# Optimization experiments

Hardware: AMD Instinct MI355X
Metric: run time of the kernel (lower is better)

The kernel has to match this reference:

```python
import jax, jax.numpy as jnp
import numpy as np
from jax import lax

ALPHA = 100.0          # SuperSpike surrogate slope (method='super', alpha=100)
DT_TAU_MEM = 0.1       # dt * tau_mem_inv = 0.001 * 100
DT_TAU_SYN = 0.2       # dt * tau_syn_inv = 0.001 * 200
V_TH = 1.0
SEQ = 40

@jax.custom_vjp
def spike(x):
    return (x > 0).astype(x.dtype)

def _spike_fwd(x):
    return (x > 0).astype(x.dtype), x

def _spike_bwd(x, g):
    # SuperSpike surrogate gradient: 1 / (alpha*|x| + 1)^2
    return (g / (ALPHA * jnp.abs(x) + 1.0) ** 2,)

spike.defvjp(_spike_fwd, _spike_bwd)

def encode(current):
    # ConstantCurrentLIFEncoder: LIF driven by constant current, SEQ steps.
    def step(v, _):
        v = v + DT_TAU_MEM * (-v + current)   # v_leak = 0
        z = spike(v - V_TH)
        v = v * (1.0 - z)                     # v_reset = 0
        return v, z
    _, zs = lax.scan(step, jnp.zeros_like(current), None, length=SEQ)
    return zs  # (SEQ, B, F)

def setup_inputs() -> dict:
    key = jax.random.key(0)
    ks = jax.random.split(key, 5)
    B = 16384
    x = jax.random.normal(ks[0], (B, 4), jnp.float32)
    w_in = jax.random.normal(ks[1], (128, 8), jnp.float32) * np.sqrt(2.0 / 8)
    w_rec = jax.random.normal(ks[2], (128, 128), jnp.float32) * np.sqrt(2.0 / 128)
    w_out = jax.random.normal(ks[3], (2, 128), jnp.float32) * np.sqrt(2.0 / 128)
    keep = jax.random.bernoulli(ks[4], 0.5, (SEQ, B, 128))
    dropout_mask = keep.astype(jnp.float32) * 2.0  # inverted dropout, p=0.5
    return {"x": x, "w_in": w_in, "w_rec": w_rec, "w_out": w_out,
            "dropout_mask": dropout_mask}

def reference(x, w_in, w_rec, w_out, dropout_mask):
    scale = 50.0
    x_pos = encode(jax.nn.relu(scale * x))     # (T, B, 4)
    x_neg = encode(jax.nn.relu(-scale * x))    # (T, B, 4)
    xs = jnp.concatenate([x_pos, x_neg], axis=2)  # (T, B, 8)

    B = x.shape[0]
    H = w_rec.shape[0]
    O = w_out.shape[0]
    z0 = jnp.zeros((B, H), x.dtype)
    v0 = jnp.zeros((B, H), x.dtype)
    i0 = jnp.zeros((B, H), x.dtype)
    vo0 = jnp.zeros((B, O), x.dtype)
    io0 = jnp.zeros((B, O), x.dtype)

    def step(carry, inp):
        z, v, i, vo, io = carry
        xt, mt = inp
        # LIFCell (recurrent)
        v_dec = v + DT_TAU_MEM * (-v + i)
        i_dec = i * (1.0 - DT_TAU_SYN)
        z_new = spike(v_dec - V_TH)
        v_new = (1.0 - z_new) * v_dec
        i_new = i_dec + xt @ w_in.T + z @ w_rec.T
        # Dropout on spikes
        z_d = z_new * mt
        # LICell readout
        vo_new = vo + DT_TAU_MEM * (-vo + io)
        io_new = io * (1.0 - DT_TAU_SYN) + z_d @ w_out.T
        return (z_new, v_new, i_new, vo_new, io_new), vo_new

    _, voltages = lax.scan(step, (z0, v0, i0, vo0, io0), (xs, dropout_mask))
    m = jnp.max(voltages, axis=0)          # (B, O)
    return jax.nn.softmax(m, axis=1)
```

## Files before the change

kernel.cpp:

```cpp
#include <hip/hip_runtime.h>
#include <cstdint>

#define T_SEQ 40
#define NB    16384
#define NH    128
#define ZSTR  168
#define GROWS 16
#define NTHR  256
#define NBLK  (NB / GROWS)

typedef float v4f __attribute__((ext_vector_type(4)));
typedef short v8s __attribute__((ext_vector_type(8)));

__device__ __forceinline__ unsigned short f2bf(float f) {
  uint32_t u = __float_as_uint(f);
  return (unsigned short)((u + 0x7FFFu + ((u >> 16) & 1u)) >> 16);
}
__device__ __forceinline__ float bf2f(unsigned short b) {
  return __uint_as_float(((uint32_t)b) << 16);
}
template <int C>
__device__ __forceinline__ float dppadd(float v) {
  int t = __builtin_amdgcn_update_dpp(0, __float_as_int(v), C, 0xF, 0xF, true);
  return v + __int_as_float(t);
}
__device__ __forceinline__ float red16(float v) {
  v = dppadd<0x111>(v);
  v = dppadd<0x112>(v);
  v = dppadd<0x114>(v);
  v = dppadd<0x118>(v);
  return v;
}

__global__ __launch_bounds__(NTHR, 2)
void Policy_22033182228693_kernel(const float* __restrict__ x,
                                  const float* __restrict__ w_in,
                                  const float* __restrict__ w_rec,
                                  const float* __restrict__ w_out,
                                  const float* __restrict__ dmask,
                                  float* __restrict__ out)
{
  __shared__ unsigned short Z[2][GROWS * ZSTR];
  __shared__ unsigned short XS[T_SEQ * 128];
  __shared__ float MB[2][GROWS * NH];
  __shared__ float UP[T_SEQ][4][GROWS][2];

  const int tid  = threadIdx.x;
  const int wv   = tid >> 6;
  const int lane = tid & 63;
  const int m    = lane & 15;
  const int q    = lane >> 4;
  const int wcol = wv * 32;
  const int gb   = blockIdx.x * GROWS;
  const size_t TS = (size_t)NB * NH;

  v8s bfr[2][5][3];
#pragma unroll
  for (int tau = 0; tau < 2; ++tau) {
    const int n = wcol + tau * 16 + m;
#pragma unroll
    for (int c = 0; c < 5; ++c) {
      const int kb = c * 32 + q * 8;
      float w8[8];
      if (c < 4) {
        float4 wa = *(const float4*)&w_rec[n * NH + kb];
        float4 wb = *(const float4*)&w_rec[n * NH + kb + 4];
        w8[0]=wa.x; w8[1]=wa.y; w8[2]=wa.z; w8[3]=wa.w;
        w8[4]=wb.x; w8[5]=wb.y; w8[6]=wb.z; w8[7]=wb.w;
      } else if (q == 0) {
        float4 wa = *(const float4*)&w_in[n * 8];
        float4 wb = *(const float4*)&w_in[n * 8 + 4];
        w8[0]=wa.x; w8[1]=wa.y; w8[2]=wa.z; w8[3]=wa.w;
        w8[4]=wb.x; w8[5]=wb.y; w8[6]=wb.z; w8[7]=wb.w;
      } else {
#pragma unroll
        for (int j = 0; j < 8; ++j) w8[j] = 0.f;
      }
      union { v8s v; unsigned short u[8]; } f0, f1, f2;
#pragma unroll
      for (int j = 0; j < 8; ++j) {
        float w = w8[j];
        unsigned short b1 = f2bf(w);  float r1 = w - bf2f(b1);
        unsigned short b2 = f2bf(r1); float r2 = r1 - bf2f(b2);
        unsigned short b3 = f2bf(r2);
        f0.u[j] = b1; f1.u[j] = b2; f2.u[j] = b3;
      }
      bfr[tau][c][0] = f0.v; bfr[tau][c][1] = f1.v; bfr[tau][c][2] = f2.v;
    }
  }

  const float wo00 = w_out[wcol + m],      wo01 = w_out[wcol + 16 + m];
  const float wo10 = w_out[NH + wcol + m], wo11 = w_out[NH + wcol + 16 + m];

  for (int e = tid; e < 2 * GROWS * ZSTR; e += NTHR) ((unsigned short*)Z)[e] = 0;
  __syncthreads();

  const int srow = tid >> 4;
  const int scol = (tid & 15) * 8;
  {
    const float* g0 = dmask + (size_t)(gb + srow) * NH + scol;
    float4 p0 = *(const float4*)g0;
    float4 p1 = *(const float4*)(g0 + 4);
    if (tid < 128) {
      const int bi = tid >> 3, ch = tid & 7;
      float xv = x[(size_t)(gb + bi) * 4 + (ch & 3)];
      float cc = fmaxf(0.f, ((ch & 4) ? -50.f : 50.f) * xv);
      float ve = 0.f;
      for (int t = 0; t < T_SEQ; ++t) {
        ve += 0.1f * (cc - ve);
        unsigned short zb = 0;
        if (ve > 1.0f) { zb = 0x3F80; ve = 0.f; }
        XS[t * 128 + tid] = zb;
        if (t == 0) Z[0][bi * ZSTR + NH + ch] = zb;
      }
    }
    float* mrow = &MB[0][srow * NH + scol];
    *(float4*)mrow = p0;
    *(float4*)(mrow + 4) = p1;
  }
  __syncthreads();

  v4f iacc[2] = {{0,0,0,0},{0,0,0,0}};
  v4f vmem[2] = {{0,0,0,0},{0,0,0,0}};
  int pb = 0;

#pragma unroll 1
  for (int t = 0; t < T_SEQ; ++t) {
    const int tn = (t + 1 < T_SEQ) ? t + 1 : T_SEQ - 1;
    const float* gs = dmask + (size_t)tn * TS + (size_t)(gb + srow) * NH + scol;
    float4 npf0 = *(const float4*)gs;
    float4 npf1 = *(const float4*)(gs + 4);

    v8s af[5];
    const unsigned short* zrow = &Z[pb][m * ZSTR];
#pragma unroll
    for (int c = 0; c < 5; ++c) af[c] = *(const v8s*)(zrow + c * 32 + q * 8);

    float zf[2][4];
#pragma unroll
    for (int tau = 0; tau < 2; ++tau) {
      v4f vd = vmem[tau] + 0.1f * (iacc[tau] - vmem[tau]);
#pragma unroll
      for (int r = 0; r < 4; ++r) {
        bool z = vd[r] > 1.0f;
        zf[tau][r] = z ? 1.0f : 0.0f;
        vmem[tau][r] = z ? 0.0f : vd[r];
      }
    }

    v4f s00 = 0.8f * iacc[0], s01 = {0,0,0,0}, s02 = {0,0,0,0};
    v4f s10 = 0.8f * iacc[1], s11 = {0,0,0,0}, s12 = {0,0,0,0};
#pragma unroll
    for (int c = 0; c < 5; ++c) {
      s00 = __builtin_amdgcn_mfma_f32_16x16x32_bf16(af[c], bfr[0][c][0], s00, 0, 0, 0);
      s10 = __builtin_amdgcn_mfma_f32_16x16x32_bf16(af[c], bfr[1][c][0], s10, 0, 0, 0);
      s01 = __builtin_amdgcn_mfma_f32_16x16x32_bf16(af[c], bfr[0][c][1], s01, 0, 0, 0);
      s11 = __builtin_amdgcn_mfma_f32_16x16x32_bf16(af[c], bfr[1][c][1], s11, 0, 0, 0);
      s02 = __builtin_amdgcn_mfma_f32_16x16x32_bf16(af[c], bfr[0][c][2], s02, 0, 0, 0);
      s12 = __builtin_amdgcn_mfma_f32_16x16x32_bf16(af[c], bfr[1][c][2], s12, 0, 0, 0);
    }
    iacc[0] = (s00 + s01) + s02;
    iacc[1] = (s10 + s11) + s12;

    unsigned short* zq = &Z[pb ^ 1][0];
#pragma unroll
    for (int tau = 0; tau < 2; ++tau)
#pragma unroll
      for (int r = 0; r < 4; ++r)
        zq[(q * 4 + r) * ZSTR + wcol + tau * 16 + m] = (zf[tau][r] != 0.f) ? 0x3F80 : 0;

    if (t + 1 < T_SEQ && tid >= 128) {
      const int u = tid - 128;
      Z[pb ^ 1][(u >> 3) * ZSTR + NH + (u & 7)] = XS[(t + 1) * 128 + u];
    }

#pragma unroll
    for (int r = 0; r < 4; ++r) {
      float mk0 = MB[t & 1][(q * 4 + r) * NH + wcol + m];
      float mk1 = MB[t & 1][(q * 4 + r) * NH + wcol + 16 + m];
      float zd0 = zf[0][r] * mk0;
      float zd1 = zf[1][r] * mk1;
      float p0 = zd0 * wo00 + zd1 * wo01;
      float p1 = zd0 * wo10 + zd1 * wo11;
      p0 = red16(p0);
      p1 = red16(p1);
      if (m == 15) {
        UP[t][wv][q * 4 + r][0] = p0;
        UP[t][wv][q * 4 + r][1] = p1;
      }
    }

    {
      float* mrow = &MB[(t + 1) & 1][srow * NH + scol];
      *(float4*)mrow = npf0;
      *(float4*)(mrow + 4) = npf1;
    }

    __syncthreads();
    pb ^= 1;
  }

  if (tid < 32) {
    const int row = tid >> 1, o = tid & 1;
    float io = 0.f, vo = 0.f, mx = -3.0e38f;
#pragma unroll 1
    for (int t = 0; t < T_SEQ; ++t) {
      float u = ((UP[t][0][row][o] + UP[t][1][row][o])
               +  UP[t][2][row][o]) + UP[t][3][row][o];
      float von = vo + 0.1f * (io - vo);
      io = 0.8f * io + u;
      vo = von;
      mx = fmaxf(mx, vo);
    }
    float other = __shfl_xor(mx, 1);
    if (o == 0) {
      float mxx = fmaxf(mx, other);
      float e0 = expf(mx - mxx), e1 = expf(other - mxx);
      float inv = 1.f / (e0 + e1);
      ((float2*)out)[gb + row] = make_float2(e0 * inv, e1 * inv);
    }
  }
}

extern "C" void kernel_launch(void* const* d_in, const int* in_sizes, int n_in,
                              void* d_out, int out_size, void* d_ws, size_t ws_size,
                              hipStream_t stream) {
  const float* x     = (const float*)d_in[0];
  const float* w_in  = (const float*)d_in[1];
  const float* w_rec = (const float*)d_in[2];
  const float* w_out = (const float*)d_in[3];
  const float* dmask = (const float*)d_in[4];
  float* out = (float*)d_out;

  hipLaunchKernelGGL(Policy_22033182228693_kernel, dim3(NBLK), dim3(NTHR), 0, stream,
                     x, w_in, w_rec, w_out, dmask, out);
}
```

Baseline: 472.4 us.

## Widen blocks to 32 rows and 8 waves, one hidden column tile per wave

Each block now handles 32 batch rows with 512 threads. Each wave owns 16 hidden columns and runs two row tiles, so the split-bf16 weight fragments held in registers are halved and the weight setup is amortised over more rows. The dropout mask is prefetched two steps ahead into a triple buffer with a padded stride, and the readout integration runs inside the step loop on wave 0 using a double-buffered partial array instead of a tail loop over all steps. The costs are more threads per barrier and fewer resident blocks per CU given the launch bound and the larger shared memory.

```diff
diff --git a/kernel.cpp b/kernel.cpp
--- a/kernel.cpp
+++ b/kernel.cpp
@@ -5,8 +5,9 @@
 #define NB    16384
 #define NH    128
 #define ZSTR  168
-#define GROWS 16
-#define NTHR  256
+#define MSTR  132
+#define GROWS 32
+#define NTHR  512
 #define NBLK  (NB / GROWS)
 
 typedef float v4f __attribute__((ext_vector_type(4)));
@@ -41,56 +42,52 @@
                                   float* __restrict__ out)
 {
   __shared__ unsigned short Z[2][GROWS * ZSTR];
-  __shared__ unsigned short XS[T_SEQ * 128];
-  __shared__ float MB[2][GROWS * NH];
-  __shared__ float UP[T_SEQ][4][GROWS][2];
+  __shared__ unsigned short XS[T_SEQ * 256];
+  __shared__ float MB[3][GROWS * MSTR];
+  __shared__ float UP[2][8][GROWS][2];
 
   const int tid  = threadIdx.x;
   const int wv   = tid >> 6;
   const int lane = tid & 63;
   const int m    = lane & 15;
   const int q    = lane >> 4;
-  const int wcol = wv * 32;
+  const int col  = wv * 16 + m;
   const int gb   = blockIdx.x * GROWS;
   const size_t TS = (size_t)NB * NH;
 
-  v8s bfr[2][5][3];
-#pragma unroll
-  for (int tau = 0; tau < 2; ++tau) {
-    const int n = wcol + tau * 16 + m;
-#pragma unroll
-    for (int c = 0; c < 5; ++c) {
-      const int kb = c * 32 + q * 8;
-      float w8[8];
-      if (c < 4) {
-        float4 wa = *(const float4*)&w_rec[n * NH + kb];
-        float4 wb = *(const float4*)&w_rec[n * NH + kb + 4];
-        w8[0]=wa.x; w8[1]=wa.y; w8[2]=wa.z; w8[3]=wa.w;
-        w8[4]=wb.x; w8[5]=wb.y; w8[6]=wb.z; w8[7]=wb.w;
-      } else if (q == 0) {
-        float4 wa = *(const float4*)&w_in[n * 8];
-        float4 wb = *(const float4*)&w_in[n * 8 + 4];
-        w8[0]=wa.x; w8[1]=wa.y; w8[2]=wa.z; w8[3]=wa.w;
-        w8[4]=wb.x; w8[5]=wb.y; w8[6]=wb.z; w8[7]=wb.w;
-      } else {
-#pragma unroll
-        for (int j = 0; j < 8; ++j) w8[j] = 0.f;
-      }
-      union { v8s v; unsigned short u[8]; } f0, f1, f2;
-#pragma unroll
-      for (int j = 0; j < 8; ++j) {
-        float w = w8[j];
-        unsigned short b1 = f2bf(w);  float r1 = w - bf2f(b1);
-        unsigned short b2 = f2bf(r1); float r2 = r1 - bf2f(b2);
-        unsigned short b3 = f2bf(r2);
-        f0.u[j] = b1; f1.u[j] = b2; f2.u[j] = b3;
-      }
-      bfr[tau][c][0] = f0.v; bfr[tau][c][1] = f1.v; bfr[tau][c][2] = f2.v;
-    }
-  }
-
-  const float wo00 = w_out[wcol + m],      wo01 = w_out[wcol + 16 + m];
-  const float wo10 = w_out[NH + wcol + m], wo11 = w_out[NH + wcol + 16 + m];
+  v8s bfr[5][3];
+#pragma unroll
+  for (int c = 0; c < 5; ++c) {
+    const int kb = c * 32 + q * 8;
+    float w8[8];
+    if (c < 4) {
+      float4 wa = *(const float4*)&w_rec[col * NH + kb];
+      float4 wb = *(const float4*)&w_rec[col * NH + kb + 4];
+      w8[0]=wa.x; w8[1]=wa.y; w8[2]=wa.z; w8[3]=wa.w;
+      w8[4]=wb.x; w8[5]=wb.y; w8[6]=wb.z; w8[7]=wb.w;
+    } else if (q == 0) {
+      float4 wa = *(const float4*)&w_in[col * 8];
+      float4 wb = *(const float4*)&w_in[col * 8 + 4];
+      w8[0]=wa.x; w8[1]=wa.y; w8[2]=wa.z; w8[3]=wa.w;
+      w8[4]=wb.x; w8[5]=wb.y; w8[6]=wb.z; w8[7]=wb.w;
+    } else {
+#pragma unroll
+      for (int j = 0; j < 8; ++j) w8[j] = 0.f;
+    }
+    union { v8s v; unsigned short u[8]; } f0, f1, f2;
+#pragma unroll
+    for (int j = 0; j < 8; ++j) {
+      float w = w8[j];
+      unsigned short b1 = f2bf(w);  float r1 = w - bf2f(b1);
+      unsigned short b2 = f2bf(r1); float r2 = r1 - bf2f(b2);
+      unsigned short b3 = f2bf(r2);
+      f0.u[j] = b1; f1.u[j] = b2; f2.u[j] = b3;
+    }
+    bfr[c][0] = f0.v; bfr[c][1] = f1.v; bfr[c][2] = f2.v;
+  }
+
+  const float wo0 = w_out[col];
+  const float wo1 = w_out[NH + col];
 
   for (int e = tid; e < 2 * GROWS * ZSTR; e += NTHR) ((unsigned short*)Z)[e] = 0;
   __syncthreads();
@@ -99,9 +96,12 @@
   const int scol = (tid & 15) * 8;
   {
     const float* g0 = dmask + (size_t)(gb + srow) * NH + scol;
-    float4 p0 = *(const float4*)g0;
-    float4 p1 = *(const float4*)(g0 + 4);
-    if (tid < 128) {
+    float4 a0 = *(const float4*)g0;
+    float4 a1 = *(const float4*)(g0 + 4);
+    const float* g1 = g0 + TS;
+    float4 b0 = *(const float4*)g1;
+    float4 b1 = *(const float4*)(g1 + 4);
+    if (tid < 256) {
       const int bi = tid >> 3, ch = tid & 7;
       float xv = x[(size_t)(gb + bi) * 4 + (ch & 3)];
       float cc = fmaxf(0.f, ((ch & 4) ? -50.f : 50.f) * xv);
@@ -110,114 +110,113 @@
         ve += 0.1f * (cc - ve);
         unsigned short zb = 0;
         if (ve > 1.0f) { zb = 0x3F80; ve = 0.f; }
-        XS[t * 128 + tid] = zb;
+        XS[t * 256 + tid] = zb;
         if (t == 0) Z[0][bi * ZSTR + NH + ch] = zb;
       }
     }
-    float* mrow = &MB[0][srow * NH + scol];
-    *(float4*)mrow = p0;
-    *(float4*)(mrow + 4) = p1;
+    float* m0 = &MB[0][srow * MSTR + scol];
+    *(float4*)m0 = a0;  *(float4*)(m0 + 4) = a1;
+    float* m1 = &MB[1][srow * MSTR + scol];
+    *(float4*)m1 = b0;  *(float4*)(m1 + 4) = b1;
   }
   __syncthreads();
 
   v4f iacc[2] = {{0,0,0,0},{0,0,0,0}};
   v4f vmem[2] = {{0,0,0,0},{0,0,0,0}};
+  float io = 0.f, vo = 0.f, mx = -3.0e38f;
+  const int lrow = lane >> 1, lo = lane & 1;
   int pb = 0;
 
 #pragma unroll 1
   for (int t = 0; t < T_SEQ; ++t) {
-    const int tn = (t + 1 < T_SEQ) ? t + 1 : T_SEQ - 1;
+    const int tn = (t + 2 < T_SEQ) ? t + 2 : T_SEQ - 1;
     const float* gs = dmask + (size_t)tn * TS + (size_t)(gb + srow) * NH + scol;
     float4 npf0 = *(const float4*)gs;
     float4 npf1 = *(const float4*)(gs + 4);
 
-    v8s af[5];
-    const unsigned short* zrow = &Z[pb][m * ZSTR];
-#pragma unroll
-    for (int c = 0; c < 5; ++c) af[c] = *(const v8s*)(zrow + c * 32 + q * 8);
-
     float zf[2][4];
 #pragma unroll
-    for (int tau = 0; tau < 2; ++tau) {
-      v4f vd = vmem[tau] + 0.1f * (iacc[tau] - vmem[tau]);
+    for (int a = 0; a < 2; ++a) {
+      v4f vd = vmem[a] + 0.1f * (iacc[a] - vmem[a]);
 #pragma unroll
       for (int r = 0; r < 4; ++r) {
         bool z = vd[r] > 1.0f;
-        zf[tau][r] = z ? 1.0f : 0.0f;
-        vmem[tau][r] = z ? 0.0f : vd[r];
+        zf[a][r] = z ? 1.0f : 0.0f;
+        vmem[a][r] = z ? 0.0f : vd[r];
       }
     }
 
-    v4f s00 = 0.8f * iacc[0], s01 = {0,0,0,0}, s02 = {0,0,0,0};
-    v4f s10 = 0.8f * iacc[1], s11 = {0,0,0,0}, s12 = {0,0,0,0};
-#pragma unroll
-    for (int c = 0; c < 5; ++c) {
-      s00 = __builtin_amdgcn_mfma_f32_16x16x32_bf16(af[c], bfr[0][c][0], s00, 0, 0, 0);
-      s10 = __builtin_amdgcn_mfma_f32_16x16x32_bf16(af[c], bfr[1][c][0], s10, 0, 0, 0);
-      s01 = __builtin_amdgcn_mfma_f32_16x16x32_bf16(af[c], bfr[0][c][1], s01, 0, 0, 0);
-      s11 = __builtin_amdgcn_mfma_f32_16x16x32_bf16(af[c], bfr[1][c][1], s11, 0, 0, 0);
-      s02 = __builtin_amdgcn_mfma_f32_16x16x32_bf16(af[c], bfr[0][c][2], s02, 0, 0, 0);
-      s12 = __builtin_amdgcn_mfma_f32_16x16x32_bf16(af[c], bfr[1][c][2], s12, 0, 0, 0);
-    }
-    iacc[0] = (s00 + s01) + s02;
-    iacc[1] = (s10 + s11) + s12;
+#pragma unroll
+    for (int a = 0; a < 2; ++a) {
+      const unsigned short* zrow = &Z[pb][(a * 16 + m) * ZSTR];
+      v8s af[5];
+#pragma unroll
+      for (int c = 0; c < 5; ++c) af[c] = *(const v8s*)(zrow + c * 32 + q * 8);
+      v4f s0 = 0.8f * iacc[a];
+      v4f s1 = {0,0,0,0}, s2 = {0,0,0,0};
+#pragma unroll
+      for (int c = 0; c < 5; ++c) {
+        s0 = __builtin_amdgcn_mfma_f32_16x16x32_bf16(af[c], bfr[c][0], s0, 0, 0, 0);
+        s1 = __builtin_amdgcn_mfma_f32_16x16x32_bf16(af[c], bfr[c][1], s1, 0, 0, 0);
+        s2 = __builtin_amdgcn_mfma_f32_16x16x32_bf16(af[c], bfr[c][2], s2, 0, 0, 0);
+      }
+      iacc[a] = (s0 + s1) + s2;
+    }
 
     unsigned short* zq = &Z[pb ^ 1][0];
 #pragma unroll
-    for (int tau = 0; tau < 2; ++tau)
+    for (int a = 0; a < 2; ++a)
 #pragma unroll
       for (int r = 0; r < 4; ++r)
-        zq[(q * 4 + r) * ZSTR + wcol + tau * 16 + m] = (zf[tau][r] != 0.f) ? 0x3F80 : 0;
-
-    if (t + 1 < T_SEQ && tid >= 128) {
-      const int u = tid - 128;
-      Z[pb ^ 1][(u >> 3) * ZSTR + NH + (u & 7)] = XS[(t + 1) * 128 + u];
-    }
-
-#pragma unroll
-    for (int r = 0; r < 4; ++r) {
-      float mk0 = MB[t & 1][(q * 4 + r) * NH + wcol + m];
-      float mk1 = MB[t & 1][(q * 4 + r) * NH + wcol + 16 + m];
-      float zd0 = zf[0][r] * mk0;
-      float zd1 = zf[1][r] * mk1;
-      float p0 = zd0 * wo00 + zd1 * wo01;
-      float p1 = zd0 * wo10 + zd1 * wo11;
-      p0 = red16(p0);
-      p1 = red16(p1);
-      if (m == 15) {
-        UP[t][wv][q * 4 + r][0] = p0;
-        UP[t][wv][q * 4 + r][1] = p1;
-      }
-    }
+        zq[(a * 16 + q * 4 + r) * ZSTR + col] = (zf[a][r] != 0.f) ? 0x3F80 : 0;
+    if (t + 1 < T_SEQ && tid < 256)
+      zq[(tid >> 3) * ZSTR + NH + (tid & 7)] = XS[(t + 1) * 256 + tid];
 
     {
-      float* mrow = &MB[(t + 1) & 1][srow * NH + scol];
+      const float* mb = MB[t % 3];
+#pragma unroll
+      for (int a = 0; a < 2; ++a)
+#pragma unroll
+        for (int r = 0; r < 4; ++r) {
+          const int row = a * 16 + q * 4 + r;
+          float zd = zf[a][r] * mb[row * MSTR + col];
+          float p0 = red16(zd * wo0);
+          float p1 = red16(zd * wo1);
+          if (m == 15) {
+            UP[t & 1][wv][row][0] = p0;
+            UP[t & 1][wv][row][1] = p1;
+          }
+        }
+    }
+
+    {
+      float* mrow = &MB[(t + 2) % 3][srow * MSTR + scol];
       *(float4*)mrow = npf0;
       *(float4*)(mrow + 4) = npf1;
     }
 
     __syncthreads();
-    pb ^= 1;
-  }
-
-  if (tid < 32) {
-    const int row = tid >> 1, o = tid & 1;
-    float io = 0.f, vo = 0.f, mx = -3.0e38f;
-#pragma unroll 1
-    for (int t = 0; t < T_SEQ; ++t) {
-      float u = ((UP[t][0][row][o] + UP[t][1][row][o])
-               +  UP[t][2][row][o]) + UP[t][3][row][o];
+
+    if (wv == 0) {
+      float u = ((UP[t & 1][0][lrow][lo] + UP[t & 1][1][lrow][lo])
+               + (UP[t & 1][2][lrow][lo] + UP[t & 1][3][lrow][lo]))
+              + ((UP[t & 1][4][lrow][lo] + UP[t & 1][5][lrow][lo])
+               + (UP[t & 1][6][lrow][lo] + UP[t & 1][7][lrow][lo]));
       float von = vo + 0.1f * (io - vo);
       io = 0.8f * io + u;
       vo = von;
       mx = fmaxf(mx, vo);
     }
+    pb ^= 1;
+  }
+
+  if (wv == 0) {
     float other = __shfl_xor(mx, 1);
-    if (o == 0) {
+    if (lo == 0) {
       float mxx = fmaxf(mx, other);
       float e0 = expf(mx - mxx), e1 = expf(other - mxx);
       float inv = 1.f / (e0 + e1);
-      ((float2*)out)[gb + row] = make_float2(e0 * inv, e1 * inv);
+      ((float2*)out)[gb + lrow] = make_float2(e0 * inv, e1 * inv);
     }
   }
 }
```

Result: no change. 474.1 us (+0.4%).
